# Kernel tuning notes

Hardware: AMD Instinct MI355X
Metric: run time of the kernel (lower is better)

## Reference

```python
import jax, jax.numpy as jnp
import numpy as np

B, T, I, H, O = 8192, 128, 28, 200, 10


def setup_inputs() -> dict:
    key = jax.random.key(0)
    ks = jax.random.split(key, 7)
    s_ih = 1.0 / np.sqrt(H)
    return {
        "x": jax.random.normal(ks[0], (B, T, I), dtype=jnp.float32),
        "W_ih": jax.random.uniform(ks[1], (H, I), jnp.float32, -s_ih, s_ih),
        "W_hh": jax.random.uniform(ks[2], (H, H), jnp.float32, -s_ih, s_ih),
        "b_ih": jax.random.uniform(ks[3], (H,), jnp.float32, -s_ih, s_ih),
        "b_hh": jax.random.uniform(ks[4], (H,), jnp.float32, -s_ih, s_ih),
        "W_fc": jax.random.uniform(ks[5], (O, H), jnp.float32, -s_ih, s_ih),
        "b_fc": jax.random.uniform(ks[6], (O,), jnp.float32, -s_ih, s_ih),
    }


def reference(x, W_ih, W_hh, b_ih, b_hh, W_fc, b_fc):
    # Precompute input projections for all timesteps in one GEMM: [B,T,H]
    xp = jnp.einsum("bti,hi->bth", x, W_ih) + b_ih + b_hh
    h0 = jnp.zeros((x.shape[0], W_hh.shape[0]), dtype=x.dtype)

    def step(h, xp_t):
        # h_t = relu(x_t W_ih^T + b_ih + h_{t-1} W_hh^T + b_hh)
        h = jax.nn.relu(xp_t + h @ W_hh.T)
        return h, None

    # scan over time: xp transposed to [T,B,H]
    h_last, _ = jax.lax.scan(step, h0, jnp.swapaxes(xp, 0, 1))
    # out[:, -1, :] then fc1
    return h_last @ W_fc.T + b_fc
```

## Files before the change

kernel.cpp:

```cpp
#include <hip/hip_runtime.h>

typedef float f4v __attribute__((ext_vector_type(4)));
typedef float f2v __attribute__((ext_vector_type(2)));
typedef short s8v __attribute__((ext_vector_type(8)));

#define TT 128
#define II 28
#define HH 200
#define BB 16
#define NT 256
#define SH 232
#define KX 224
#define CH 8
#define XW (CH * BB * II)

__device__ __forceinline__ unsigned pk_hu(float a, float b) {
    unsigned ua = __builtin_bit_cast(unsigned, a) + 0x8000u;
    unsigned ub = __builtin_bit_cast(unsigned, b) + 0x8000u;
    return __builtin_amdgcn_perm(ub, ua, 0x07060302);
}
__device__ __forceinline__ short f2bf(float f) {
    return (short)((__builtin_bit_cast(unsigned, f) + 0x8000u) >> 16);
}

__global__ __launch_bounds__(NT, 2)
void rnn_r7(const float* __restrict__ x,
            const float* __restrict__ W_ih,
            const float* __restrict__ W_hh,
            const float* __restrict__ b_ih,
            const float* __restrict__ b_hh,
            const float* __restrict__ W_fc,
            const float* __restrict__ b_fc,
            float* __restrict__ out)
{
    __shared__ __align__(16) short Hs[2][BB][SH];
    __shared__ __align__(16) float Xl[2][XW + 8];

    const int tid  = threadIdx.x;
    const int lane = tid & 63;
    const int q    = lane >> 4;
    const int lr   = lane & 15;
    const int wave = tid >> 6;
    const int b0   = blockIdx.x * BB;

    const int first = (wave == 0) ? 0 : 1 + 3 * wave;
    const int cnt   = (wave == 0) ? 4 : 3;

    for (int i = tid; i < 2 * BB * SH / 2; i += NT) ((int*)Hs)[i] = 0;

    s8v Af[4][8];
    #pragma unroll
    for (int u = 0; u < 4; ++u) {
        const int j = 16 * (first + u) + lr;
        #pragma unroll
        for (int kc = 0; kc < 8; ++kc) {
            union { short s[8]; s8v v; } tv;
            #pragma unroll
            for (int i = 0; i < 8; ++i) {
                const int k = 32 * kc + 8 * q + i;
                float w = 0.0f;
                if (u < cnt && j < HH) {
                    if (k < HH)                    w = W_hh[j * HH + k];
                    else if (k >= KX && k < KX+II) w = W_ih[j * II + (k - KX)];
                }
                tv.s[i] = f2bf(w);
            }
            Af[u][kc] = tv.v;
        }
    }

    f4v biasv[4];
    #pragma unroll
    for (int u = 0; u < 4; ++u) {
        f4v bv = {0.f, 0.f, 0.f, 0.f};
        #pragma unroll
        for (int i = 0; i < 4; ++i) {
            const int j = 16 * (first + u) + 4 * q + i;
            if (u < cnt && j < HH) bv[i] = b_ih[j] + b_hh[j];
        }
        biasv[u] = bv;
    }

    const int wv = wave - 2;
    long xoff[7];
    #pragma unroll
    for (int e = 0; e < 7; ++e) {
        if (wv >= 0) {
            const int m  = ((wv * 7 + e) << 6) + lane;
            const int tl = m / 112;
            const int rm = m - tl * 112;
            const int r  = rm / 7;
            const int c4 = rm - r * 7;
            xoff[e] = ((long)(b0 + r) * TT + tl) * II + c4 * 4;
        } else xoff[e] = 0;
    }
    auto load_chunk = [&](int cc) {
        if (wv >= 0) {
            float* dbase = &Xl[cc & 1][(wv * 7) * 256];
            #pragma unroll
            for (int e = 0; e < 7; ++e) {
                const float* src = x + xoff[e] + (long)cc * (CH * II);
                __builtin_amdgcn_global_load_lds(
                    (const __attribute__((address_space(1))) void*)src,
                    (__attribute__((address_space(3))) void*)(dbase + e * 256),
                    16, 0, 0);
            }
        }
    };

    load_chunk(0);
    __syncthreads();

    for (int c = 0; c < TT / CH; ++c) {
        if (c + 1 < TT / CH) load_chunk(c + 1);
        #pragma unroll
        for (int s = 0; s < CH; ++s) {
            const int t  = c * CH + s;
            const int pb = t & 1;

            s8v bf[7];
            #pragma unroll
            for (int kc = 0; kc < 7; ++kc)
                bf[kc] = *(const s8v*)&Hs[pb][lr][32 * kc + 8 * q];

            const float* xr = &Xl[c & 1][s * (BB * II) + lr * II + 8 * q];
            const f2v x0 = *(const f2v*)(xr + 0);
            const f2v x1 = *(const f2v*)(xr + 2);
            const f2v x2 = *(const f2v*)(xr + 4);
            const f2v x3 = *(const f2v*)(xr + 6);
            union { unsigned u4[4]; s8v v; } xf;
            xf.u4[0] = pk_hu(x0.x, x0.y);
            xf.u4[1] = pk_hu(x1.x, x1.y);
            xf.u4[2] = pk_hu(x2.x, x2.y);
            xf.u4[3] = pk_hu(x3.x, x3.y);

            f4v acc[4];
            #pragma unroll
            for (int u = 0; u < 4; ++u)
                if (u < cnt)
                    acc[u] = __builtin_amdgcn_mfma_f32_16x16x32_bf16(Af[u][7], xf.v, biasv[u], 0, 0, 0);
            #pragma unroll
            for (int kc = 0; kc < 7; ++kc) {
                #pragma unroll
                for (int u = 0; u < 4; ++u)
                    if (u < cnt)
                        acc[u] = __builtin_amdgcn_mfma_f32_16x16x32_bf16(Af[u][kc], bf[kc], acc[u], 0, 0, 0);
            }

            #pragma unroll
            for (int u = 0; u < 4; ++u) {
                if (u < cnt) {
                    const int jt = first + u;
                    const float r0 = fmaxf(acc[u].x, 0.f), r1 = fmaxf(acc[u].y, 0.f);
                    const float r2 = fmaxf(acc[u].z, 0.f), r3 = fmaxf(acc[u].w, 0.f);
                    int2 hv;
                    hv.x = (int)pk_hu(r0, r1);
                    hv.y = (int)pk_hu(r2, r3);
                    *(int2*)&Hs[pb ^ 1][lr][16 * jt + 4 * q] = hv;
                }
            }
            __syncthreads();
        }
    }

    if (tid < BB * 10) {
        const int o = tid >> 4, r = tid & 15;
        float sacc = b_fc[o];
        for (int k = 0; k < HH; ++k) {
            const float hk = __builtin_bit_cast(float,
                (unsigned)((unsigned short)Hs[0][r][k]) << 16);
            sacc = fmaf(hk, W_fc[o * HH + k], sacc);
        }
        __builtin_nontemporal_store(sacc, &out[(long)(b0 + r) * 10 + o]);
    }
}

extern "C" void kernel_launch(void* const* d_in, const int* in_sizes, int n_in,
                              void* d_out, int out_size, void* d_ws, size_t ws_size,
                              hipStream_t stream) {
    const float* x    = (const float*)d_in[0];
    const float* W_ih = (const float*)d_in[1];
    const float* W_hh = (const float*)d_in[2];
    const float* b_ih = (const float*)d_in[3];
    const float* b_hh = (const float*)d_in[4];
    const float* W_fc = (const float*)d_in[5];
    const float* b_fc = (const float*)d_in[6];
    float* out = (float*)d_out;

    rnn_r7<<<dim3(8192 / BB), dim3(NT), 0, stream>>>(
        x, W_ih, W_hh, b_ih, b_hh, W_fc, b_fc, out);
}
```

Measured before the change: 302.3 us.

## Run each batch tile's recurrence in a single wave without block barriers

Changes the kernel from four waves sharing the hidden-state update to one 64-lane wave per 16-row batch tile. That wave holds all 13 output tiles of W_hh/W_ih in registers, so the per-timestep __syncthreads and the double-buffered hidden state go away. The bias is folded into the weight matrix through a constant-one column in the hidden buffer. The H fragment for the next k-chunk is prefetched while the current MFMAs issue. The cost is a very large register footprint (13x8 weight fragments plus 13 accumulators), only one wave per block, and possible spilling or low occupancy. It also relies on in-place hidden-state writes being ordered after the reads within one wave.

```diff
diff --git a/kernel.cpp b/kernel.cpp
--- a/kernel.cpp
+++ b/kernel.cpp
@@ -8,9 +8,7 @@
 #define II 28
 #define HH 200
 #define BB 16
-#define NT 256
 #define SH 232
-#define KX 224
 #define CH 8
 #define XW (CH * BB * II)
 
@@ -23,8 +21,8 @@
     return (short)((__builtin_bit_cast(unsigned, f) + 0x8000u) >> 16);
 }
 
-__global__ __launch_bounds__(NT, 2)
-void rnn_r7(const float* __restrict__ x,
+__global__ __launch_bounds__(64, 1)
+void rnn_pw(const float* __restrict__ x,
             const float* __restrict__ W_ih,
             const float* __restrict__ W_hh,
             const float* __restrict__ b_ih,
@@ -33,25 +31,21 @@
             const float* __restrict__ b_fc,
             float* __restrict__ out)
 {
-    __shared__ __align__(16) short Hs[2][BB][SH];
+    __shared__ __align__(16) short Hs[BB][SH];
     __shared__ __align__(16) float Xl[2][XW + 8];
 
-    const int tid  = threadIdx.x;
-    const int lane = tid & 63;
+    const int lane = threadIdx.x & 63;
     const int q    = lane >> 4;
     const int lr   = lane & 15;
-    const int wave = tid >> 6;
     const int b0   = blockIdx.x * BB;
 
-    const int first = (wave == 0) ? 0 : 1 + 3 * wave;
-    const int cnt   = (wave == 0) ? 4 : 3;
+    for (int i = lane; i < BB * SH / 2; i += 64) ((int*)Hs)[i] = 0;
+    if (lane < BB) Hs[lane][208] = (short)0x3F80;
 
-    for (int i = tid; i < 2 * BB * SH / 2; i += NT) ((int*)Hs)[i] = 0;
-
-    s8v Af[4][8];
+    s8v Af[13][8];
     #pragma unroll
-    for (int u = 0; u < 4; ++u) {
-        const int j = 16 * (first + u) + lr;
+    for (int u = 0; u < 13; ++u) {
+        const int j = 16 * u + lr;
         #pragma unroll
         for (int kc = 0; kc < 8; ++kc) {
             union { short s[8]; s8v v; } tv;
@@ -59,9 +53,10 @@
             for (int i = 0; i < 8; ++i) {
                 const int k = 32 * kc + 8 * q + i;
                 float w = 0.0f;
-                if (u < cnt && j < HH) {
-                    if (k < HH)                    w = W_hh[j * HH + k];
-                    else if (k >= KX && k < KX+II) w = W_ih[j * II + (k - KX)];
+                if (j < HH) {
+                    if (k < HH)                     w = W_hh[j * HH + k];
+                    else if (k == 208)              w = b_ih[j] + b_hh[j];
+                    else if (k >= 224 && k < 252)   w = W_ih[j * II + (k - 224)];
                 }
                 tv.s[i] = f2bf(w);
             }
@@ -69,60 +64,37 @@
         }
     }
 
-    f4v biasv[4];
+    long xoff[14];
     #pragma unroll
-    for (int u = 0; u < 4; ++u) {
-        f4v bv = {0.f, 0.f, 0.f, 0.f};
-        #pragma unroll
-        for (int i = 0; i < 4; ++i) {
-            const int j = 16 * (first + u) + 4 * q + i;
-            if (u < cnt && j < HH) bv[i] = b_ih[j] + b_hh[j];
-        }
-        biasv[u] = bv;
-    }
-
-    const int wv = wave - 2;
-    long xoff[7];
-    #pragma unroll
-    for (int e = 0; e < 7; ++e) {
-        if (wv >= 0) {
-            const int m  = ((wv * 7 + e) << 6) + lane;
-            const int tl = m / 112;
-            const int rm = m - tl * 112;
-            const int r  = rm / 7;
-            const int c4 = rm - r * 7;
-            xoff[e] = ((long)(b0 + r) * TT + tl) * II + c4 * 4;
-        } else xoff[e] = 0;
+    for (int e = 0; e < 14; ++e) {
+        const int m  = (e << 6) + lane;
+        const int tl = m / 112;
+        const int rm = m - tl * 112;
+        const int r  = rm / 7;
+        const int c4 = rm - r * 7;
+        xoff[e] = ((long)(b0 + r) * TT + tl) * II + c4 * 4;
     }
     auto load_chunk = [&](int cc) {
-        if (wv >= 0) {
-            float* dbase = &Xl[cc & 1][(wv * 7) * 256];
-            #pragma unroll
-            for (int e = 0; e < 7; ++e) {
-                const float* src = x + xoff[e] + (long)cc * (CH * II);
-                __builtin_amdgcn_global_load_lds(
-                    (const __attribute__((address_space(1))) void*)src,
-                    (__attribute__((address_space(3))) void*)(dbase + e * 256),
-                    16, 0, 0);
-            }
+        float* dbase = &Xl[cc & 1][0];
+        #pragma unroll
+        for (int e = 0; e < 14; ++e) {
+            const float* src = x + xoff[e] + (long)cc * (CH * II);
+            __builtin_amdgcn_global_load_lds(
+                (const __attribute__((address_space(1))) void*)src,
+                (__attribute__((address_space(3))) void*)(dbase + e * 256),
+                16, 0, 0);
         }
     };
 
     load_chunk(0);
-    __syncthreads();
+
+    const f4v zero = {0.f, 0.f, 0.f, 0.f};
 
     for (int c = 0; c < TT / CH; ++c) {
+        __builtin_amdgcn_s_waitcnt(0);
         if (c + 1 < TT / CH) load_chunk(c + 1);
-        #pragma unroll
+
         for (int s = 0; s < CH; ++s) {
-            const int t  = c * CH + s;
-            const int pb = t & 1;
-
-            s8v bf[7];
-            #pragma unroll
-            for (int kc = 0; kc < 7; ++kc)
-                bf[kc] = *(const s8v*)&Hs[pb][lr][32 * kc + 8 * q];
-
             const float* xr = &Xl[c & 1][s * (BB * II) + lr * II + 8 * q];
             const f2v x0 = *(const f2v*)(xr + 0);
             const f2v x1 = *(const f2v*)(xr + 2);
@@ -134,41 +106,39 @@
             xf.u4[2] = pk_hu(x2.x, x2.y);
             xf.u4[3] = pk_hu(x3.x, x3.y);
 
-            f4v acc[4];
+            s8v cur = *(const s8v*)&Hs[lr][8 * q];
+            f4v acc[13];
             #pragma unroll
-            for (int u = 0; u < 4; ++u)
-                if (u < cnt)
-                    acc[u] = __builtin_amdgcn_mfma_f32_16x16x32_bf16(Af[u][7], xf.v, biasv[u], 0, 0, 0);
+            for (int u = 0; u < 13; ++u)
+                acc[u] = __builtin_amdgcn_mfma_f32_16x16x32_bf16(Af[u][7], xf.v, zero, 0, 0, 0);
             #pragma unroll
             for (int kc = 0; kc < 7; ++kc) {
+                s8v nxt;
+                if (kc < 6) nxt = *(const s8v*)&Hs[lr][32 * (kc + 1) + 8 * q];
                 #pragma unroll
-                for (int u = 0; u < 4; ++u)
-                    if (u < cnt)
-                        acc[u] = __builtin_amdgcn_mfma_f32_16x16x32_bf16(Af[u][kc], bf[kc], acc[u], 0, 0, 0);
+                for (int u = 0; u < 13; ++u)
+                    acc[u] = __builtin_amdgcn_mfma_f32_16x16x32_bf16(Af[u][kc], cur, acc[u], 0, 0, 0);
+                if (kc < 6) cur = nxt;
             }
 
             #pragma unroll
-            for (int u = 0; u < 4; ++u) {
-                if (u < cnt) {
-                    const int jt = first + u;
-                    const float r0 = fmaxf(acc[u].x, 0.f), r1 = fmaxf(acc[u].y, 0.f);
-                    const float r2 = fmaxf(acc[u].z, 0.f), r3 = fmaxf(acc[u].w, 0.f);
-                    int2 hv;
-                    hv.x = (int)pk_hu(r0, r1);
-                    hv.y = (int)pk_hu(r2, r3);
-                    *(int2*)&Hs[pb ^ 1][lr][16 * jt + 4 * q] = hv;
-                }
+            for (int u = 0; u < 13; ++u) {
+                const float r0 = fmaxf(acc[u].x, 0.f), r1 = fmaxf(acc[u].y, 0.f);
+                const float r2 = fmaxf(acc[u].z, 0.f), r3 = fmaxf(acc[u].w, 0.f);
+                int2 hv;
+                hv.x = (int)pk_hu(r0, r1);
+                hv.y = (int)pk_hu(r2, r3);
+                *(int2*)&Hs[lr][16 * u + 4 * q] = hv;
             }
-            __syncthreads();
         }
     }
 
-    if (tid < BB * 10) {
-        const int o = tid >> 4, r = tid & 15;
+    for (int i = lane; i < BB * 10; i += 64) {
+        const int o = i >> 4, r = i & 15;
         float sacc = b_fc[o];
         for (int k = 0; k < HH; ++k) {
             const float hk = __builtin_bit_cast(float,
-                (unsigned)((unsigned short)Hs[0][r][k]) << 16);
+                (unsigned)((unsigned short)Hs[r][k]) << 16);
             sacc = fmaf(hk, W_fc[o * HH + k], sacc);
         }
         __builtin_nontemporal_store(sacc, &out[(long)(b0 + r) * 10 + o]);
@@ -187,6 +157,6 @@
     const float* b_fc = (const float*)d_in[6];
     float* out = (float*)d_out;
 
-    rnn_r7<<<dim3(8192 / BB), dim3(NT), 0, stream>>>(
+    rnn_pw<<<dim3(8192 / BB), dim3(64), 0, stream>>>(
         x, W_ih, W_hh, b_ih, b_hh, W_fc, b_fc, out);
 }
```

After: 486.8 us. +61.0%, slower.
